# Optimization experiments

Hardware: AMD Instinct MI355X
Metric: run time of the kernel (lower is better)

Reference implementation:

```python
import math
import jax, jax.numpy as jnp
import numpy as np

B, T, D = 4, 2048, 1024
H = 16
HD = D // H  # 64

def setup_inputs() -> dict:
    key = jax.random.key(0)
    k1, k2, k3 = jax.random.split(key, 3)
    x = jax.random.normal(k1, (B, T, D), dtype=jnp.float32)
    # weights stored as [in, out]; equivalent to torch Linear weight [out,in] transposed
    w_qkv = jax.random.normal(k2, (D, 3 * D), dtype=jnp.float32) * (1.0 / math.sqrt(D))
    w_out = jax.random.normal(k3, (D, D), dtype=jnp.float32) * (1.0 / math.sqrt(D))
    return {"x": x, "w_qkv": w_qkv, "w_out": w_out}

def reference(x, w_qkv, w_out):
    b, t, c = x.shape
    hd = c // H
    qkv = x @ w_qkv                                   # [B,T,3C]
    q, k, v = jnp.split(qkv, 3, axis=-1)
    # [B,T,C] -> [B,H,T,hd]
    q = q.reshape(b, t, H, hd).transpose(0, 2, 1, 3)
    k = k.reshape(b, t, H, hd).transpose(0, 2, 1, 3)
    v = v.reshape(b, t, H, hd).transpose(0, 2, 1, 3)
    scale = 1.0 / math.sqrt(hd)
    scores = jnp.einsum('bhqd,bhkd->bhqk', q, k) * scale  # [B,H,T,T]
    causal = jnp.tril(jnp.ones((t, t), dtype=bool))
    scores = jnp.where(causal, scores, jnp.finfo(scores.dtype).min)
    attn = jax.nn.softmax(scores, axis=-1)
    out = jnp.einsum('bhqk,bhkd->bhqd', attn, v)       # [B,H,T,hd]
    out = out.transpose(0, 2, 1, 3).reshape(b, t, c)
    return out @ w_out
```

## Files before the change

### kernel.cpp

```cpp
#include <hip/hip_runtime.h>
#include <stdint.h>
#include <stddef.h>

#define BB 4
#define TT 2048
#define DD 1024
#define HH 16
#define HDIM 64
#define BT (BB*TT)
#define N1 (3*DD)

typedef __attribute__((ext_vector_type(8))) short short8;
typedef __attribute__((ext_vector_type(4))) float floatx4;
typedef __attribute__((ext_vector_type(4))) unsigned short ushortx4;
typedef __attribute__((ext_vector_type(2))) unsigned int uint2v;

__device__ __forceinline__ unsigned short f2b(float f) {
    unsigned int u = __float_as_uint(f);
    u += 0x7fffu + ((u >> 16) & 1u);
    return (unsigned short)(u >> 16);
}

__device__ __forceinline__ unsigned int cvtpk(float a, float b) {
    unsigned int r;
    asm("v_cvt_pk_bf16_f32 %0, %1, %2" : "=v"(r) : "v"(a), "v"(b));
    return r;
}

__device__ __forceinline__ void gld_lds16(const void* g, void* l) {
    __builtin_amdgcn_global_load_lds(
        (__attribute__((address_space(1))) void*)(g),
        (__attribute__((address_space(3))) void*)(l), 16, 0, 0);
}

__global__ void cvt_bf16(const float* __restrict__ src, unsigned short* __restrict__ dst, int n4) {
    int i = blockIdx.x * blockDim.x + threadIdx.x;
    if (i < n4) {
        floatx4 f = ((const floatx4*)src)[i];
        ushortx4 o;
        o.x = f2b(f.x); o.y = f2b(f.y); o.z = f2b(f.z); o.w = f2b(f.w);
        ((ushortx4*)dst)[i] = o;
    }
}

__global__ void transpose_cvt(const float* __restrict__ src, unsigned short* __restrict__ dst,
                              int R, int C) {
    __shared__ float tile[32][33];
    const int c0 = blockIdx.x * 32, r0 = blockIdx.y * 32;
    const int x = threadIdx.x, y = threadIdx.y;
    for (int yy = y; yy < 32; yy += 8)
        tile[yy][x] = src[(size_t)(r0 + yy) * C + c0 + x];
    __syncthreads();
    for (int yy = y; yy < 32; yy += 8)
        dst[(size_t)(c0 + yy) * R + r0 + x] = f2b(tile[x][yy]);
}

__global__ __launch_bounds__(256, 2)
void gemm_qkv(const unsigned short* __restrict__ A,
              const unsigned short* __restrict__ Bt,
              unsigned short* __restrict__ Cout, int M, int N, int K,
              float qscale, unsigned short* __restrict__ vt_out) {
    __shared__ unsigned short a_tile[2][256 * 32];
    __shared__ unsigned short b_tile[2][192 * 32];
    const int tid  = threadIdx.x;
    const int wave = tid >> 6;
    const int lane = tid & 63;
    const int quad = lane >> 4;
    const int lc   = lane & 15;
    const int wm = wave >> 1, wn = wave & 1;
    const int row0 = blockIdx.y * 256;
    const int col0 = blockIdx.x * 192;

    const int r_in = lane >> 2;
    const int kseg = (lane & 3) * 8;
    const unsigned short* gA0 = A  + (size_t)(row0 + (wave     ) * 16 + r_in) * K + kseg;
    const unsigned short* gA1 = A  + (size_t)(row0 + (wave +  4) * 16 + r_in) * K + kseg;
    const unsigned short* gA2 = A  + (size_t)(row0 + (wave +  8) * 16 + r_in) * K + kseg;
    const unsigned short* gA3 = A  + (size_t)(row0 + (wave + 12) * 16 + r_in) * K + kseg;
    const unsigned short* gB0 = Bt + (size_t)(col0 + (wave     ) * 16 + r_in) * K + kseg;
    const unsigned short* gB1 = Bt + (size_t)(col0 + (wave +  4) * 16 + r_in) * K + kseg;
    const unsigned short* gB2 = Bt + (size_t)(col0 + (wave +  8) * 16 + r_in) * K + kseg;
    const int sA0 = (wave     ) * 512, sA1 = (wave +  4) * 512;
    const int sA2 = (wave +  8) * 512, sA3 = (wave + 12) * 512;

    floatx4 acc[8][6];
    #pragma unroll
    for (int i = 0; i < 8; i++)
        #pragma unroll
        for (int j = 0; j < 6; j++)
            acc[i][j] = (floatx4){0.f, 0.f, 0.f, 0.f};

    gld_lds16(gA0, &a_tile[0][sA0]);
    gld_lds16(gA1, &a_tile[0][sA1]);
    gld_lds16(gA2, &a_tile[0][sA2]);
    gld_lds16(gA3, &a_tile[0][sA3]);
    gld_lds16(gB0, &b_tile[0][sA0]);
    gld_lds16(gB1, &b_tile[0][sA1]);
    gld_lds16(gB2, &b_tile[0][sA2]);
    int buf = 0;

    const int nkt = K >> 5;
    for (int kt = 0; kt < nkt; ++kt) {
        __syncthreads();
        if (kt + 1 < nkt) {
            gA0 += 32; gA1 += 32; gA2 += 32; gA3 += 32;
            gB0 += 32; gB1 += 32; gB2 += 32;
            gld_lds16(gA0, &a_tile[buf ^ 1][sA0]);
            gld_lds16(gA1, &a_tile[buf ^ 1][sA1]);
            gld_lds16(gA2, &a_tile[buf ^ 1][sA2]);
            gld_lds16(gA3, &a_tile[buf ^ 1][sA3]);
            gld_lds16(gB0, &b_tile[buf ^ 1][sA0]);
            gld_lds16(gB1, &b_tile[buf ^ 1][sA1]);
            gld_lds16(gB2, &b_tile[buf ^ 1][sA2]);
        }

        short8 bf[6];
        #pragma unroll
        for (int ni = 0; ni < 6; ++ni)
            bf[ni] = *(const short8*)&b_tile[buf][(wn * 96 + ni * 16 + lc) * 32 + quad * 8];
        #pragma unroll
        for (int mi = 0; mi < 8; ++mi) {
            short8 af = *(const short8*)&a_tile[buf][(wm * 128 + mi * 16 + lc) * 32 + quad * 8];
            #pragma unroll
            for (int ni = 0; ni < 6; ++ni)
                acc[mi][ni] = __builtin_amdgcn_mfma_f32_16x16x32_bf16(af, bf[ni], acc[mi][ni], 0, 0, 0);
        }
        buf ^= 1;
    }

    #pragma unroll
    for (int mi = 0; mi < 8; ++mi) {
        const int rbase = row0 + wm * 128 + mi * 16 + quad * 4;
        #pragma unroll
        for (int ni = 0; ni < 6; ++ni) {
            const int colbase = col0 + wn * 96 + ni * 16;
            const int col = colbase + lc;
            if (colbase < 2 * DD) {
                const float sc = (colbase < DD) ? qscale : 1.0f;
                #pragma unroll
                for (int r = 0; r < 4; ++r)
                    Cout[(size_t)(rbase + r) * N + col] = f2b(acc[mi][ni][r] * sc);
            } else {
                const int vcol = col - 2 * DD;
                const int hh = vcol >> 6, d = vcol & 63;
                const int bq = rbase >> 11, t = rbase & 2047;
                uint2v pk;
                pk.x = cvtpk(acc[mi][ni][0], acc[mi][ni][1]);
                pk.y = cvtpk(acc[mi][ni][2], acc[mi][ni][3]);
                *(uint2v*)&vt_out[(size_t)((bq * 16 + hh) * 64 + d) * TT + t] = pk;
            }
        }
    }
}

__global__ __launch_bounds__(256, 3)
void gemm_out(const unsigned short* __restrict__ A,
              const unsigned short* __restrict__ Bt,
              float* __restrict__ Cout, int M, int N, int K) {
    __shared__ unsigned short a_tile[2][128 * 32];
    __shared__ unsigned short b_tile[2][128 * 32];
    const int tid  = threadIdx.x;
    const int wave = tid >> 6;
    const int lane = tid & 63;
    const int quad = lane >> 4;
    const int lc   = lane & 15;
    const int wm = wave >> 1, wn = wave & 1;
    const int row0 = blockIdx.y * 128;
    const int col0 = blockIdx.x * 128;

    const int c0 = wave, c1 = wave + 4;
    const int r_in = lane >> 2;
    const int kseg = (lane & 3) * 8;
    const unsigned short* gA0 = A  + (size_t)(row0 + c0 * 16 + r_in) * K + kseg;
    const unsigned short* gA1 = A  + (size_t)(row0 + c1 * 16 + r_in) * K + kseg;
    const unsigned short* gB0 = Bt + (size_t)(col0 + c0 * 16 + r_in) * K + kseg;
    const unsigned short* gB1 = Bt + (size_t)(col0 + c1 * 16 + r_in) * K + kseg;
    const int sA0 = c0 * 512, sA1 = c1 * 512;

    floatx4 acc[4][4];
    #pragma unroll
    for (int i = 0; i < 4; i++)
        #pragma unroll
        for (int j = 0; j < 4; j++)
            acc[i][j] = (floatx4){0.f, 0.f, 0.f, 0.f};

    gld_lds16(gA0, &a_tile[0][sA0]);
    gld_lds16(gA1, &a_tile[0][sA1]);
    gld_lds16(gB0, &b_tile[0][sA0]);
    gld_lds16(gB1, &b_tile[0][sA1]);
    int buf = 0;

    const int nkt = K >> 5;
    for (int kt = 0; kt < nkt; ++kt) {
        __syncthreads();
        if (kt + 1 < nkt) {
            gA0 += 32; gA1 += 32; gB0 += 32; gB1 += 32;
            gld_lds16(gA0, &a_tile[buf ^ 1][sA0]);
            gld_lds16(gA1, &a_tile[buf ^ 1][sA1]);
            gld_lds16(gB0, &b_tile[buf ^ 1][sA0]);
            gld_lds16(gB1, &b_tile[buf ^ 1][sA1]);
        }

        short8 af[4], bf[4];
        #pragma unroll
        for (int mi = 0; mi < 4; ++mi)
            af[mi] = *(const short8*)&a_tile[buf][(wm * 64 + mi * 16 + lc) * 32 + quad * 8];
        #pragma unroll
        for (int ni = 0; ni < 4; ++ni)
            bf[ni] = *(const short8*)&b_tile[buf][(wn * 64 + ni * 16 + lc) * 32 + quad * 8];
        #pragma unroll
        for (int mi = 0; mi < 4; ++mi)
            #pragma unroll
            for (int ni = 0; ni < 4; ++ni)
                acc[mi][ni] = __builtin_amdgcn_mfma_f32_16x16x32_bf16(af[mi], bf[ni], acc[mi][ni], 0, 0, 0);
        buf ^= 1;
    }

    #pragma unroll
    for (int mi = 0; mi < 4; ++mi) {
        const int rbase = row0 + wm * 64 + mi * 16 + quad * 4;
        #pragma unroll
        for (int ni = 0; ni < 4; ++ni) {
            const int col = col0 + wn * 64 + ni * 16 + lc;
            #pragma unroll
            for (int r = 0; r < 4; ++r)
                Cout[(size_t)(rbase + r) * N + col] = acc[mi][ni][r];
        }
    }
}

__global__ __launch_bounds__(256, 2)
void attn_fwd(const unsigned short* __restrict__ qkv,
              const unsigned short* __restrict__ vt,
              unsigned short* __restrict__ out) {
    __shared__ unsigned short kbuf[2][64 * 64];
    __shared__ unsigned short vbuf[2][64 * 64];
    __shared__ unsigned short p_lds[4][32 * 72];
    const int bh = blockIdx.x;
    const int b = bh >> 4, h = bh & 15;
    const int pr = blockIdx.y;
    const int tid = threadIdx.x;
    const int wave = tid >> 6, lane = tid & 63;
    const int quad = lane >> 4, lc = lane & 15;
    unsigned short* pw = p_lds[wave];

    const int sr = wave * 8 + (lane >> 3);
    const int lg = (lane & 7) ^ (sr & 7);
    const unsigned short* ksrc0 = qkv + (size_t)(b * TT + sr) * N1 + DD + h * HDIM + lg * 8;
    const unsigned short* vsrc0 = vt + (size_t)(bh * HDIM + sr) * TT + lg * 8;
    const int stg = wave * 512;

    int fofs[4][2];
    #pragma unroll
    for (int mi = 0; mi < 4; ++mi)
        #pragma unroll
        for (int kk = 0; kk < 2; ++kk)
            fofs[mi][kk] = (mi * 16 + lc) * 64 + (((kk * 4 + quad) ^ (lc & 7)) * 8);

    gld_lds16(ksrc0, &kbuf[0][stg]);
    gld_lds16(ksrc0 + 32 * (size_t)N1, &kbuf[0][stg + 2048]);
    gld_lds16(vsrc0, &vbuf[0][stg]);
    gld_lds16(vsrc0 + 32 * (size_t)TT, &vbuf[0][stg + 2048]);
    int buf = 0;

    for (int pass = 0; pass < 2; ++pass) {
        const int j = pass ? (15 - pr) : pr;
        const int q0 = j * 128;
        const int r0 = q0 + wave * 32;
        const int tmax = 2 * j + 1;

        short8 qf[2][2];
        #pragma unroll
        for (int ni = 0; ni < 2; ++ni)
            #pragma unroll
            for (int kk = 0; kk < 2; ++kk)
                qf[ni][kk] = *(const short8*)(qkv + (size_t)(b * TT + r0 + ni * 16 + lc) * N1 + h * HDIM + kk * 32 + quad * 8);

        float lp[2] = {0.f, 0.f};
        floatx4 o_acc[4][2];
        #pragma unroll
        for (int mi = 0; mi < 4; ++mi)
            #pragma unroll
            for (int ni = 0; ni < 2; ++ni)
                o_acc[mi][ni] = (floatx4){0.f, 0.f, 0.f, 0.f};

        for (int t = 0; t <= tmax; ++t) {
            const int kv0 = t * 64;
            __syncthreads();

            const int nt = (t < tmax) ? (t + 1) : (pass == 0 ? 0 : -1);
            if (nt >= 0) {
                const unsigned short* ks = ksrc0 + (size_t)nt * 64 * N1;
                const unsigned short* vs = vsrc0 + nt * 64;
                gld_lds16(ks, &kbuf[buf ^ 1][stg]);
                gld_lds16(ks + 32 * (size_t)N1, &kbuf[buf ^ 1][stg + 2048]);
                gld_lds16(vs, &vbuf[buf ^ 1][stg]);
                gld_lds16(vs + 32 * (size_t)TT, &vbuf[buf ^ 1][stg + 2048]);
            }

            short8 kf[4][2];
            #pragma unroll
            for (int mi = 0; mi < 4; ++mi)
                #pragma unroll
                for (int kk = 0; kk < 2; ++kk)
                    kf[mi][kk] = *(const short8*)&kbuf[buf][fofs[mi][kk]];
            floatx4 sa[4][2];
            #pragma unroll
            for (int mi = 0; mi < 4; ++mi)
                #pragma unroll
                for (int ni = 0; ni < 2; ++ni) {
                    floatx4 z = (floatx4){0.f, 0.f, 0.f, 0.f};
                    z = __builtin_amdgcn_mfma_f32_16x16x32_bf16(kf[mi][0], qf[ni][0], z, 0, 0, 0);
                    z = __builtin_amdgcn_mfma_f32_16x16x32_bf16(kf[mi][1], qf[ni][1], z, 0, 0, 0);
                    sa[mi][ni] = z;
                }

            if (kv0 + 63 > r0) {
                #pragma unroll
                for (int ni = 0; ni < 2; ++ni) {
                    const int qg = r0 + ni * 16 + lc;
                    #pragma unroll
                    for (int mi = 0; mi < 4; ++mi) {
                        const int kvb = kv0 + mi * 16 + quad * 4;
                        #pragma unroll
                        for (int r = 0; r < 4; ++r)
                            sa[mi][ni][r] = (kvb + r <= qg) ? sa[mi][ni][r] : -1e30f;
                    }
                }
            }

            #pragma unroll
            for (int ni = 0; ni < 2; ++ni) {
                float rs = 0.f;
                #pragma unroll
                for (int mi = 0; mi < 4; ++mi) {
                    float p0 = __builtin_amdgcn_exp2f(sa[mi][ni][0]);
                    float p1 = __builtin_amdgcn_exp2f(sa[mi][ni][1]);
                    float p2 = __builtin_amdgcn_exp2f(sa[mi][ni][2]);
                    float p3 = __builtin_amdgcn_exp2f(sa[mi][ni][3]);
                    rs += (p0 + p1) + (p2 + p3);
                    uint2v pk;
                    pk.x = cvtpk(p0, p1);
                    pk.y = cvtpk(p2, p3);
                    *(uint2v*)&pw[(ni * 16 + lc) * 72 + mi * 16 + quad * 4] = pk;
                }
                lp[ni] += rs;
            }

            short8 pf[2][2];
            #pragma unroll
            for (int ni = 0; ni < 2; ++ni)
                #pragma unroll
                for (int kk = 0; kk < 2; ++kk)
                    pf[ni][kk] = *(const short8*)&pw[(ni * 16 + lc) * 72 + kk * 32 + quad * 8];
            short8 vf[4][2];
            #pragma unroll
            for (int mi = 0; mi < 4; ++mi)
                #pragma unroll
                for (int kk = 0; kk < 2; ++kk)
                    vf[mi][kk] = *(const short8*)&vbuf[buf][fofs[mi][kk]];
            #pragma unroll
            for (int mi = 0; mi < 4; ++mi)
                #pragma unroll
                for (int ni = 0; ni < 2; ++ni) {
                    o_acc[mi][ni] = __builtin_amdgcn_mfma_f32_16x16x32_bf16(vf[mi][0], pf[ni][0], o_acc[mi][ni], 0, 0, 0);
                    o_acc[mi][ni] = __builtin_amdgcn_mfma_f32_16x16x32_bf16(vf[mi][1], pf[ni][1], o_acc[mi][ni], 0, 0, 0);
                }

            buf ^= 1;
        }

        #pragma unroll
        for (int ni = 0; ni < 2; ++ni) {
            float lt = lp[ni];
            lt += __shfl_xor(lt, 16);
            lt += __shfl_xor(lt, 32);
            const float inv = 1.0f / lt;
            const size_t tok = (size_t)(b * TT + r0 + ni * 16 + lc);
            #pragma unroll
            for (int mi = 0; mi < 4; ++mi) {
                uint2v pk;
                pk.x = cvtpk(o_acc[mi][ni][0] * inv, o_acc[mi][ni][1] * inv);
                pk.y = cvtpk(o_acc[mi][ni][2] * inv, o_acc[mi][ni][3] * inv);
                *(uint2v*)&out[tok * DD + h * HDIM + mi * 16 + quad * 4] = pk;
            }
        }
    }
}

extern "C" void kernel_launch(void* const* d_in, const int* in_sizes, int n_in,
                              void* d_out, int out_size, void* d_ws, size_t ws_size,
                              hipStream_t stream) {
    const float* x     = (const float*)d_in[0];
    const float* w_qkv = (const float*)d_in[1];
    const float* w_out = (const float*)d_in[2];
    float* out = (float*)d_out;

    unsigned short* ws  = (unsigned short*)d_ws;
    unsigned short* xb  = ws;
    unsigned short* qkv = xb  + (size_t)BT * DD;
    unsigned short* wqT = qkv + (size_t)BT * N1;
    unsigned short* woT = wqT + (size_t)N1 * DD;
    unsigned short* vtb = woT + (size_t)DD * DD;

    const float QSCALE = 0.18033688011112042f;

    cvt_bf16<<<(BT * DD / 4 + 255) / 256, 256, 0, stream>>>(x, xb, BT * DD / 4);
    transpose_cvt<<<dim3(N1 / 32, DD / 32), dim3(32, 8), 0, stream>>>(w_qkv, wqT, DD, N1);
    transpose_cvt<<<dim3(DD / 32, DD / 32), dim3(32, 8), 0, stream>>>(w_out, woT, DD, DD);
    gemm_qkv<<<dim3(N1 / 192, BT / 256), 256, 0, stream>>>(xb, wqT, qkv, BT, N1, DD, QSCALE, vtb);
    attn_fwd<<<dim3(BB * HH, 8), 256, 0, stream>>>(qkv, vtb, xb);
    gemm_out<<<dim3(DD / 128, BT / 128), 256, 0, stream>>>(xb, woT, out, BT, DD, DD);
}
```

Baseline: 239.2 us.

## Restructure QKV GEMM into 8-wave, 64-wide K pipeline with swizzled LDS

The QKV projection GEMM now runs 512 threads (8 waves) per block with a K-step of 64 instead of 32. Global-to-LDS prefetches are split across four compute phases separated by barriers, with s_setprio raised around the MFMA bursts. LDS columns are XOR-swizzled to avoid bank conflicts. The aim is to overlap loads with MFMA and halve the loop iterations, at the cost of doubled LDS usage (about 112 KB per block) and more barriers, which may limit occupancy.

```diff
diff --git a/kernel.cpp b/kernel.cpp
--- a/kernel.cpp
+++ b/kernel.cpp
@@ -55,85 +55,137 @@
         dst[(size_t)(c0 + yy) * R + r0 + x] = f2b(tile[x][yy]);
 }
 
-__global__ __launch_bounds__(256, 2)
+__global__ __launch_bounds__(512, 2)
 void gemm_qkv(const unsigned short* __restrict__ A,
               const unsigned short* __restrict__ Bt,
               unsigned short* __restrict__ Cout, int M, int N, int K,
               float qscale, unsigned short* __restrict__ vt_out) {
-    __shared__ unsigned short a_tile[2][256 * 32];
-    __shared__ unsigned short b_tile[2][192 * 32];
+    __shared__ unsigned short a_tile[2][256 * 64];
+    __shared__ unsigned short b_tile[2][192 * 64];
     const int tid  = threadIdx.x;
     const int wave = tid >> 6;
     const int lane = tid & 63;
     const int quad = lane >> 4;
     const int lc   = lane & 15;
-    const int wm = wave >> 1, wn = wave & 1;
+    const int wm = wave >> 2, wn = wave & 3;
     const int row0 = blockIdx.y * 256;
     const int col0 = blockIdx.x * 192;
 
-    const int r_in = lane >> 2;
-    const int kseg = (lane & 3) * 8;
-    const unsigned short* gA0 = A  + (size_t)(row0 + (wave     ) * 16 + r_in) * K + kseg;
-    const unsigned short* gA1 = A  + (size_t)(row0 + (wave +  4) * 16 + r_in) * K + kseg;
-    const unsigned short* gA2 = A  + (size_t)(row0 + (wave +  8) * 16 + r_in) * K + kseg;
-    const unsigned short* gA3 = A  + (size_t)(row0 + (wave + 12) * 16 + r_in) * K + kseg;
-    const unsigned short* gB0 = Bt + (size_t)(col0 + (wave     ) * 16 + r_in) * K + kseg;
-    const unsigned short* gB1 = Bt + (size_t)(col0 + (wave +  4) * 16 + r_in) * K + kseg;
-    const unsigned short* gB2 = Bt + (size_t)(col0 + (wave +  8) * 16 + r_in) * K + kseg;
-    const int sA0 = (wave     ) * 512, sA1 = (wave +  4) * 512;
-    const int sA2 = (wave +  8) * 512, sA3 = (wave + 12) * 512;
-
-    floatx4 acc[8][6];
+    const int srow = lane >> 3;
+    const int scol = ((lane & 7) ^ srow) * 8;
+    const unsigned short* aS = A  + (size_t)(row0 + wave * 8 + srow) * K + scol;
+    const unsigned short* bS = Bt + (size_t)(col0 + wave * 8 + srow) * K + scol;
+    const size_t rstep = (size_t)64 * K;
+    const int aL = wave * 8 * 64;
+
+    int arow[8], brow[3];
+    #pragma unroll
+    for (int mi = 0; mi < 8; ++mi) arow[mi] = (wm * 128 + mi * 16 + lc) * 64;
+    #pragma unroll
+    for (int ni = 0; ni < 3; ++ni) brow[ni] = (wn * 48 + ni * 16 + lc) * 64;
+    const int sx0 = ((quad    ) ^ (lc & 7)) * 8;
+    const int sx1 = ((quad + 4) ^ (lc & 7)) * 8;
+
+    floatx4 acc[8][3];
     #pragma unroll
     for (int i = 0; i < 8; i++)
         #pragma unroll
-        for (int j = 0; j < 6; j++)
+        for (int j = 0; j < 3; j++)
             acc[i][j] = (floatx4){0.f, 0.f, 0.f, 0.f};
 
-    gld_lds16(gA0, &a_tile[0][sA0]);
-    gld_lds16(gA1, &a_tile[0][sA1]);
-    gld_lds16(gA2, &a_tile[0][sA2]);
-    gld_lds16(gA3, &a_tile[0][sA3]);
-    gld_lds16(gB0, &b_tile[0][sA0]);
-    gld_lds16(gB1, &b_tile[0][sA1]);
-    gld_lds16(gB2, &b_tile[0][sA2]);
-    int buf = 0;
-
-    const int nkt = K >> 5;
-    for (int kt = 0; kt < nkt; ++kt) {
-        __syncthreads();
-        if (kt + 1 < nkt) {
-            gA0 += 32; gA1 += 32; gA2 += 32; gA3 += 32;
-            gB0 += 32; gB1 += 32; gB2 += 32;
-            gld_lds16(gA0, &a_tile[buf ^ 1][sA0]);
-            gld_lds16(gA1, &a_tile[buf ^ 1][sA1]);
-            gld_lds16(gA2, &a_tile[buf ^ 1][sA2]);
-            gld_lds16(gA3, &a_tile[buf ^ 1][sA3]);
-            gld_lds16(gB0, &b_tile[buf ^ 1][sA0]);
-            gld_lds16(gB1, &b_tile[buf ^ 1][sA1]);
-            gld_lds16(gB2, &b_tile[buf ^ 1][sA2]);
-        }
-
-        short8 bf[6];
-        #pragma unroll
-        for (int ni = 0; ni < 6; ++ni)
-            bf[ni] = *(const short8*)&b_tile[buf][(wn * 96 + ni * 16 + lc) * 32 + quad * 8];
-        #pragma unroll
-        for (int mi = 0; mi < 8; ++mi) {
-            short8 af = *(const short8*)&a_tile[buf][(wm * 128 + mi * 16 + lc) * 32 + quad * 8];
-            #pragma unroll
-            for (int ni = 0; ni < 6; ++ni)
-                acc[mi][ni] = __builtin_amdgcn_mfma_f32_16x16x32_bf16(af, bf[ni], acc[mi][ni], 0, 0, 0);
-        }
-        buf ^= 1;
+    #pragma unroll
+    for (int i = 0; i < 4; ++i) gld_lds16(aS + i * rstep, &a_tile[0][aL + i * 4096]);
+    #pragma unroll
+    for (int i = 0; i < 3; ++i) gld_lds16(bS + i * rstep, &b_tile[0][aL + i * 4096]);
+
+    const int nkt = K >> 6;
+    size_t ko = 64;
+    for (int t = 0; t < nkt; ++t) {
+        const int db = t & 1;
+        const unsigned short* at = &a_tile[db][0];
+        const unsigned short* bt = &b_tile[db][0];
+        unsigned short* an = &a_tile[db ^ 1][0];
+        unsigned short* bn = &b_tile[db ^ 1][0];
+        const bool pre = (t + 1 < nkt);
+
+        short8 bf[3][2], af[4];
+
+        if (pre) {
+            gld_lds16(aS + ko,         &an[aL]);
+            gld_lds16(aS + rstep + ko, &an[aL + 4096]);
+            asm volatile("s_waitcnt vmcnt(2)" ::: "memory");
+        } else {
+            asm volatile("s_waitcnt vmcnt(0)" ::: "memory");
+        }
+        __builtin_amdgcn_s_barrier();
+        __builtin_amdgcn_sched_barrier(0);
+        #pragma unroll
+        for (int ni = 0; ni < 3; ++ni) bf[ni][0] = *(const short8*)&bt[brow[ni] + sx0];
+        #pragma unroll
+        for (int mi = 0; mi < 4; ++mi) af[mi] = *(const short8*)&at[arow[mi] + sx0];
+        __builtin_amdgcn_s_setprio(1);
+        #pragma unroll
+        for (int mi = 0; mi < 4; ++mi)
+            #pragma unroll
+            for (int ni = 0; ni < 3; ++ni)
+                acc[mi][ni] = __builtin_amdgcn_mfma_f32_16x16x32_bf16(af[mi], bf[ni][0], acc[mi][ni], 0, 0, 0);
+        __builtin_amdgcn_s_setprio(0);
+        __builtin_amdgcn_s_barrier();
+
+        if (pre) {
+            gld_lds16(aS + 2 * rstep + ko, &an[aL + 2 * 4096]);
+            gld_lds16(aS + 3 * rstep + ko, &an[aL + 3 * 4096]);
+        }
+        #pragma unroll
+        for (int ni = 0; ni < 3; ++ni) bf[ni][1] = *(const short8*)&bt[brow[ni] + sx1];
+        #pragma unroll
+        for (int mi = 0; mi < 4; ++mi) af[mi] = *(const short8*)&at[arow[mi] + sx1];
+        __builtin_amdgcn_s_setprio(1);
+        #pragma unroll
+        for (int mi = 0; mi < 4; ++mi)
+            #pragma unroll
+            for (int ni = 0; ni < 3; ++ni)
+                acc[mi][ni] = __builtin_amdgcn_mfma_f32_16x16x32_bf16(af[mi], bf[ni][1], acc[mi][ni], 0, 0, 0);
+        __builtin_amdgcn_s_setprio(0);
+        __builtin_amdgcn_s_barrier();
+
+        if (pre) {
+            gld_lds16(bS + ko,             &bn[aL]);
+            gld_lds16(bS + rstep + ko,     &bn[aL + 4096]);
+            gld_lds16(bS + 2 * rstep + ko, &bn[aL + 2 * 4096]);
+        }
+        #pragma unroll
+        for (int mi = 0; mi < 4; ++mi) af[mi] = *(const short8*)&at[arow[mi + 4] + sx0];
+        __builtin_amdgcn_s_setprio(1);
+        #pragma unroll
+        for (int mi = 0; mi < 4; ++mi)
+            #pragma unroll
+            for (int ni = 0; ni < 3; ++ni)
+                acc[mi + 4][ni] = __builtin_amdgcn_mfma_f32_16x16x32_bf16(af[mi], bf[ni][0], acc[mi + 4][ni], 0, 0, 0);
+        __builtin_amdgcn_s_setprio(0);
+        __builtin_amdgcn_s_barrier();
+
+        #pragma unroll
+        for (int mi = 0; mi < 4; ++mi) af[mi] = *(const short8*)&at[arow[mi + 4] + sx1];
+        __builtin_amdgcn_s_setprio(1);
+        #pragma unroll
+        for (int mi = 0; mi < 4; ++mi)
+            #pragma unroll
+            for (int ni = 0; ni < 3; ++ni)
+                acc[mi + 4][ni] = __builtin_amdgcn_mfma_f32_16x16x32_bf16(af[mi], bf[ni][1], acc[mi + 4][ni], 0, 0, 0);
+        __builtin_amdgcn_s_setprio(0);
+        __builtin_amdgcn_s_barrier();
+        __builtin_amdgcn_sched_barrier(0);
+
+        ko += 64;
     }
 
     #pragma unroll
     for (int mi = 0; mi < 8; ++mi) {
         const int rbase = row0 + wm * 128 + mi * 16 + quad * 4;
         #pragma unroll
-        for (int ni = 0; ni < 6; ++ni) {
-            const int colbase = col0 + wn * 96 + ni * 16;
+        for (int ni = 0; ni < 3; ++ni) {
+            const int colbase = col0 + wn * 48 + ni * 16;
             const int col = colbase + lc;
             if (colbase < 2 * DD) {
                 const float sc = (colbase < DD) ? qscale : 1.0f;
@@ -143,11 +195,11 @@
             } else {
                 const int vcol = col - 2 * DD;
                 const int hh = vcol >> 6, d = vcol & 63;
-                const int bq = rbase >> 11, t = rbase & 2047;
+                const int bq = rbase >> 11, tt = rbase & 2047;
                 uint2v pk;
                 pk.x = cvtpk(acc[mi][ni][0], acc[mi][ni][1]);
                 pk.y = cvtpk(acc[mi][ni][2], acc[mi][ni][3]);
-                *(uint2v*)&vt_out[(size_t)((bq * 16 + hh) * 64 + d) * TT + t] = pk;
+                *(uint2v*)&vt_out[(size_t)((bq * 16 + hh) * 64 + d) * TT + tt] = pk;
             }
         }
     }
@@ -408,7 +460,7 @@
     cvt_bf16<<<(BT * DD / 4 + 255) / 256, 256, 0, stream>>>(x, xb, BT * DD / 4);
     transpose_cvt<<<dim3(N1 / 32, DD / 32), dim3(32, 8), 0, stream>>>(w_qkv, wqT, DD, N1);
     transpose_cvt<<<dim3(DD / 32, DD / 32), dim3(32, 8), 0, stream>>>(w_out, woT, DD, DD);
-    gemm_qkv<<<dim3(N1 / 192, BT / 256), 256, 0, stream>>>(xb, wqT, qkv, BT, N1, DD, QSCALE, vtb);
+    gemm_qkv<<<dim3(N1 / 192, BT / 256), 512, 0, stream>>>(xb, wqT, qkv, BT, N1, DD, QSCALE, vtb);
     attn_fwd<<<dim3(BB * HH, 8), 256, 0, stream>>>(qkv, vtb, xb);
     gemm_out<<<dim3(DD / 128, BT / 128), 256, 0, stream>>>(xb, woT, out, BT, DD, DD);
 }
```

New measurement: 255.8 us. +6.9%, slower.
